# Kernel tuning notes

Measured on AMD Instinct MI355X. Metric: run time of the kernel, lower is better.

## Reference

```python
import jax, jax.numpy as jnp
from jax import lax
import numpy as np

D_MODEL = 256
NQ = 256          # nqueries / npoint
RADIUS = 0.3
NSAMPLE = 16
EPS = 1e-5


def _conv1d(x, W, b):  # x: (B,C,N), W: (O,C)
    return jnp.einsum('bcn,oc->bon', x, W) + b[None, :, None]


def _bn1d(x, g, be):  # train-mode batchnorm over (B, N)
    m = x.mean(axis=(0, 2), keepdims=True)
    v = x.var(axis=(0, 2), keepdims=True)
    return g[None, :, None] * (x - m) * lax.rsqrt(v + EPS) + be[None, :, None]


def _bn2d(x, g, be):  # x: (B,C,Q,S)
    m = x.mean(axis=(0, 2, 3), keepdims=True)
    v = x.var(axis=(0, 2, 3), keepdims=True)
    return g[None, :, None, None] * (x - m) * lax.rsqrt(v + EPS) + be[None, :, None, None]


def _fps(xyz, nq):
    # sequential farthest point sampling, starts at index 0 (matches CUDA impl)
    B, N, _ = xyz.shape

    def step(carry, _):
        dist, far = carry
        centroid = jnp.take_along_axis(xyz, far[:, None, None], axis=1)  # (B,1,3)
        d = jnp.sum((xyz - centroid) ** 2, axis=-1)                      # (B,N)
        dist = jnp.minimum(dist, d)
        nxt = jnp.argmax(dist, axis=-1).astype(jnp.int32)
        return (dist, nxt), far

    init = (jnp.full((B, N), 1e10, xyz.dtype), jnp.zeros((B,), jnp.int32))
    _, inds = lax.scan(step, init, None, length=nq)
    return inds.T  # (B,nq)


def _ball_query(query_xyz, xyz, radius, nsample):
    # query_xyz: (B,Q,3), xyz: (B,N,3) -> idx (B,Q,nsample) int32
    N = xyz.shape[1]
    d2 = jnp.sum((query_xyz[:, :, None, :] - xyz[:, None, :, :]) ** 2, axis=-1)  # (B,Q,N)
    within = d2 < radius * radius
    scores = jnp.where(within, jnp.arange(N, dtype=jnp.int32), jnp.int32(N))
    neg_top, _ = lax.top_k(-scores, nsample)          # nsample smallest scores, in order
    idx = -neg_top                                    # (B,Q,nsample)
    cnt = within.sum(axis=-1)                         # (B,Q)
    first = jnp.where(cnt > 0, idx[..., 0], 0)        # fill value (first neighbor, else 0)
    valid = jnp.arange(nsample) < cnt[..., None]
    return jnp.where(valid, idx, first[..., None])


def setup_inputs() -> dict:
    key = jax.random.key(0)
    ks = jax.random.split(key, 32)
    B, N, C = 16, 4096, D_MODEL
    s = 0.02
    inp = {
        'encode_xyz': jax.random.uniform(ks[0], (B, N, 3), jnp.float32),
        'encode_features': jax.random.normal(ks[1], (B, C, N), jnp.float32),
        # FFN_vote: conv1 -> bn -> relu -> conv2 -> bn -> relu -> conv3
        'W1': jax.random.normal(ks[2], (C, C), jnp.float32) * s,
        'b1': jnp.zeros((C,), jnp.float32),
        'g1': jnp.ones((C,), jnp.float32),
        'be1': jnp.zeros((C,), jnp.float32),
        'W2': jax.random.normal(ks[3], (C, C), jnp.float32) * s,
        'b2': jnp.zeros((C,), jnp.float32),
        'g2': jnp.ones((C,), jnp.float32),
        'be2': jnp.zeros((C,), jnp.float32),
        'W3': jax.random.normal(ks[4], (3 + C, C), jnp.float32) * s,
        'b3': jnp.zeros((3 + C,), jnp.float32),
        # SA module shared MLP (conv2d 1x1): (C+3)->C->C->C, each with BN2d
        'mW1': jax.random.normal(ks[5], (C, C + 3), jnp.float32) * s,
        'mb1': jnp.zeros((C,), jnp.float32),
        'mg1': jnp.ones((C,), jnp.float32),
        'mbe1': jnp.zeros((C,), jnp.float32),
        'mW2': jax.random.normal(ks[6], (C, C), jnp.float32) * s,
        'mb2': jnp.zeros((C,), jnp.float32),
        'mg2': jnp.ones((C,), jnp.float32),
        'mbe2': jnp.zeros((C,), jnp.float32),
        'mW3': jax.random.normal(ks[7], (C, C), jnp.float32) * s,
        'mb3': jnp.zeros((C,), jnp.float32),
        'mg3': jnp.ones((C,), jnp.float32),
        'mbe3': jnp.zeros((C,), jnp.float32),
    }
    return inp


def reference(encode_xyz, encode_features, W1, b1, g1, be1, W2, b2, g2, be2, W3, b3,
              mW1, mb1, mg1, mbe1, mW2, mb2, mg2, mbe2, mW3, mb3, mg3, mbe3):
    B, N, _ = encode_xyz.shape

    # FFN_vote
    h = jax.nn.relu(_bn1d(_conv1d(encode_features, W1, b1), g1, be1))
    h = jax.nn.relu(_bn1d(_conv1d(h, W2, b2), g2, be2))
    out = _conv1d(h, W3, b3)                      # (B, 3+C, N)

    coord_shift = jnp.clip(jax.nn.sigmoid(out[:, :3, :]), 0.1, 0.9)
    vote_xyz = encode_xyz + coord_shift.transpose(0, 2, 1) - 0.5   # (B,N,3)

    feat = encode_features + out[:, 3:, :]
    feat = feat / jnp.linalg.norm(feat, axis=1, keepdims=True)     # L2 normalize over C

    sample_inds = _fps(encode_xyz, NQ)                             # (B,NQ) int32

    # SA module: gather new centers from vote_xyz at FPS inds
    query_xyz = jnp.take_along_axis(vote_xyz, sample_inds[:, :, None], axis=1)  # (B,NQ,3)

    idx = _ball_query(query_xyz, vote_xyz, RADIUS, NSAMPLE)        # (B,NQ,NS)
    bidx = jnp.arange(B)[:, None, None]
    grouped_xyz = (vote_xyz[bidx, idx] - query_xyz[:, :, None, :]) / RADIUS  # (B,NQ,NS,3)
    grouped_feat = feat.transpose(0, 2, 1)[bidx, idx]                         # (B,NQ,NS,C)
    g = jnp.concatenate([grouped_xyz, grouped_feat], axis=-1)                 # (B,NQ,NS,3+C)
    g = g.transpose(0, 3, 1, 2)                                               # (B,3+C,NQ,NS)

    g = jax.nn.relu(_bn2d(jnp.einsum('bcqs,oc->boqs', g, mW1) + mb1[None, :, None, None], mg1, mbe1))
    g = jax.nn.relu(_bn2d(jnp.einsum('bcqs,oc->boqs', g, mW2) + mb2[None, :, None, None], mg2, mbe2))
    g = jax.nn.relu(_bn2d(jnp.einsum('bcqs,oc->boqs', g, mW3) + mb3[None, :, None, None], mg3, mbe3))
    query_features = jnp.max(g, axis=-1)                                      # (B,C,NQ)

    return vote_xyz, encode_xyz, sample_inds, query_xyz, query_features
```

## Files before the change

kernel.cpp:

```cpp
#include <hip/hip_runtime.h>
#include <math.h>

#define NPT 4096
#define NB 16

typedef short v8s __attribute__((ext_vector_type(8)));
typedef float v4f __attribute__((ext_vector_type(4)));

__device__ __forceinline__ float dist2e(float x, float y, float z,
                                        float cx, float cy, float cz) {
    float dx = __fsub_rn(x, cx), dy = __fsub_rn(y, cy), dz = __fsub_rn(z, cz);
    return __fadd_rn(__fadd_rn(__fmul_rn(dx, dx), __fmul_rn(dy, dy)), __fmul_rn(dz, dz));
}

__device__ __forceinline__ unsigned long long packdi(float v, int n) {
    return ((unsigned long long)__float_as_uint(v) << 32) |
           (unsigned long long)(0xFFFFFFFFu - (unsigned)n);
}

__device__ __forceinline__ unsigned short f2bf(float f) {
    unsigned u = __float_as_uint(f);
    u = u + 0x7FFFu + ((u >> 16) & 1u);
    return (unsigned short)(u >> 16);
}

__device__ __forceinline__ unsigned pk2(float a, float b) {
    unsigned r;
    asm("v_cvt_pk_bf16_f32 %0, %1, %2" : "=v"(r) : "v"(a), "v"(b));
    return r;
}

__device__ __forceinline__ uint2 split2(float a, float b) {
    unsigned h = pk2(a, b);
    float ra = __uint_as_float(h << 16);
    float rb = __uint_as_float(h & 0xFFFF0000u);
    unsigned l = pk2(a - ra, b - rb);
    return make_uint2(h, l);
}

template <int CTRL>
__device__ __forceinline__ float dpp_maxf(float v) {
    int o = __builtin_amdgcn_update_dpp(__float_as_int(v), __float_as_int(v),
                                        CTRL, 0xF, 0xF, false);
    return fmaxf(v, __int_as_float(o));
}
template <int CTRL>
__device__ __forceinline__ unsigned dpp_maxu(unsigned v) {
    unsigned o = (unsigned)__builtin_amdgcn_update_dpp((int)v, (int)v,
                                                       CTRL, 0xF, 0xF, false);
    return v > o ? v : o;
}

__device__ void fps_seg(const float* __restrict__ xyz, int b, int it0, int it1,
                        int* __restrict__ inds_i, float* __restrict__ inds_f,
                        float* __restrict__ dws, int* __restrict__ farws,
                        char* scr) {
    unsigned long long (*s_red)[4] = (unsigned long long (*)[4])scr;
    const int t = threadIdx.x;
    const int lane = t & 63, wid = t >> 6;
    const float* pb = xyz + (size_t)b * NPT * 3;
    float px[16], py[16], pz[16], d[16];
    #pragma unroll
    for (int j = 0; j < 16; ++j) {
        int p = j * 256 + t;
        px[j] = pb[p * 3 + 0];
        py[j] = pb[p * 3 + 1];
        pz[j] = pb[p * 3 + 2];
    }
    int far;
    if (it0 == 0) {
        #pragma unroll
        for (int j = 0; j < 16; ++j) d[j] = 1e10f;
        far = 0;
    } else {
        #pragma unroll
        for (int j = 0; j < 16; ++j) d[j] = dws[b * 4096 + j * 256 + t];
        far = farws[b];
    }
    for (int it = it0; it < it1; ++it) {
        const int par = it & 1;
        if (t == 0) { inds_i[it] = far; inds_f[it] = (float)far; }
        const float cx = pb[far * 3 + 0];
        const float cy = pb[far * 3 + 1];
        const float cz = pb[far * 3 + 2];
        d[0] = fminf(d[0], dist2e(px[0], py[0], pz[0], cx, cy, cz));
        unsigned long long best = packdi(d[0], t);
        #pragma unroll
        for (int j = 1; j < 16; ++j) {
            d[j] = fminf(d[j], dist2e(px[j], py[j], pz[j], cx, cy, cz));
            unsigned long long c = packdi(d[j], j * 256 + t);
            if (c > best) best = c;
        }
        const unsigned hi = (unsigned)(best >> 32);
        const unsigned lo = (unsigned)(best & 0xFFFFFFFFull);
        float m = __uint_as_float(hi);
        m = dpp_maxf<0x111>(m);
        m = dpp_maxf<0x112>(m);
        m = dpp_maxf<0x114>(m);
        m = dpp_maxf<0x118>(m);
        m = dpp_maxf<0x142>(m);
        m = dpp_maxf<0x143>(m);
        const unsigned mbits = (unsigned)__builtin_amdgcn_readlane(__float_as_int(m), 63);
        unsigned cand = (hi == mbits) ? lo : 0u;
        cand = dpp_maxu<0x111>(cand);
        cand = dpp_maxu<0x112>(cand);
        cand = dpp_maxu<0x114>(cand);
        cand = dpp_maxu<0x118>(cand);
        cand = dpp_maxu<0x142>(cand);
        cand = dpp_maxu<0x143>(cand);
        const unsigned wlo = (unsigned)__builtin_amdgcn_readlane((int)cand, 63);
        if (lane == 0)
            s_red[par][wid] = ((unsigned long long)mbits << 32) | (unsigned long long)wlo;
        __syncthreads();
        unsigned long long mm = s_red[par][0];
        if (s_red[par][1] > mm) mm = s_red[par][1];
        if (s_red[par][2] > mm) mm = s_red[par][2];
        if (s_red[par][3] > mm) mm = s_red[par][3];
        far = (int)(0xFFFFFFFFu - (unsigned)(mm & 0xFFFFFFFFull));
    }
    if (it1 < 256) {
        #pragma unroll
        for (int j = 0; j < 16; ++j) dws[b * 4096 + j * 256 + t] = d[j];
        if (t == 0) farws[b] = far;
    }
}

template <bool PRE_BN, bool STATS>
__global__ __launch_bounds__(256, 4)
void fgemm_k(const float* __restrict__ X,
             const unsigned short* __restrict__ Wh,
             const unsigned short* __restrict__ Wl,
             const float* __restrict__ bias,
             const float* __restrict__ scl, const float* __restrict__ sft,
             float* __restrict__ Y,
             float* __restrict__ psum, float* __restrict__ psqr,
             const float* __restrict__ xyz, int* __restrict__ sinds,
             float* __restrict__ inds_f, float* __restrict__ fpsd,
             int* __restrict__ fpsfar, int it0, int it1) {
    __shared__ __align__(16) unsigned short sBh[128 * 64];
    __shared__ __align__(16) unsigned short sBl[128 * 64];
    if (blockIdx.x < 16) {
        fps_seg(xyz, blockIdx.x, it0, it1, sinds + blockIdx.x * 256,
                inds_f + blockIdx.x * 256, fpsd, fpsfar, (char*)sBh);
        return;
    }
    int idx = blockIdx.x - 16;
    idx = (idx & 7) * 128 + (idx >> 3);
    const int b = idx >> 6, rem = idx & 63;
    const int nt = rem >> 1;
    const int n0 = nt * 128, o0 = (rem & 1) * 128;
    const int t = threadIdx.x;
    const int w = t >> 6, lane = t & 63;
    const int wm = (w >> 1) * 64, wn = (w & 1) * 64;
    const int lr = lane & 15, lk = lane >> 4;
    char* cBh = (char*)sBh;
    char* cBl = (char*)sBl;

    v4f acc[4][4];
    v4f zz = {0.f, 0.f, 0.f, 0.f};
    #pragma unroll
    for (int i = 0; i < 4; ++i)
        #pragma unroll
        for (int j = 0; j < 4; ++j) acc[i][j] = zz;

    const size_t aoff = (size_t)(o0 + wm + lr) * 256 + lk * 8;
    const unsigned short* pah = Wh + aoff;
    const unsigned short* pal = Wl + aoff;

    const int cblk = t >> 5, nq = t & 31;
    const float* xb = X + ((size_t)b * 256 + cblk * 8) * 4096 + n0 + nq * 4;

    #pragma unroll 1
    for (int ks = 0; ks < 4; ++ks) {
        const int k0 = ks * 64;
        v4f xv[8];
        #pragma unroll
        for (int i = 0; i < 8; ++i)
            xv[i] = *(const v4f*)(xb + (size_t)(k0 + i) * 4096);
        if (PRE_BN) {
            const v4f s0 = *(const v4f*)(scl + k0 + cblk * 8);
            const v4f s1 = *(const v4f*)(scl + k0 + cblk * 8 + 4);
            const v4f f0 = *(const v4f*)(sft + k0 + cblk * 8);
            const v4f f1 = *(const v4f*)(sft + k0 + cblk * 8 + 4);
            #pragma unroll
            for (int i = 0; i < 8; ++i) {
                const float si = (i < 4) ? s0[i] : s1[i - 4];
                const float fi = (i < 4) ? f0[i] : f1[i - 4];
                #pragma unroll
                for (int j = 0; j < 4; ++j)
                    xv[i][j] = fmaxf(fmaf(xv[i][j], si, fi), 0.f);
            }
        }
        __syncthreads();
        #pragma unroll
        for (int j = 0; j < 4; ++j) {
            const int n = nq * 4 + j;
            uint2 p0 = split2(xv[0][j], xv[1][j]);
            uint2 p1 = split2(xv[2][j], xv[3][j]);
            uint2 p2 = split2(xv[4][j], xv[5][j]);
            uint2 p3 = split2(xv[6][j], xv[7][j]);
            uint4 hh, ll;
            hh.x = p0.x; hh.y = p1.x; hh.z = p2.x; hh.w = p3.x;
            ll.x = p0.y; ll.y = p1.y; ll.z = p2.y; ll.w = p3.y;
            const int ad = n * 128 + ((cblk * 16) ^ ((n & 7) << 4));
            *(uint4*)(cBh + ad) = hh;
            *(uint4*)(cBl + ad) = ll;
        }
        __syncthreads();
        #pragma unroll
        for (int kb = 0; kb < 2; ++kb) {
            const int koff = kb * 64 + lk * 16;
            const int ka = k0 + kb * 32;
            v8s ahf[4], alf[4], bhf[4], blf[4];
            #pragma unroll
            for (int f = 0; f < 4; ++f) {
                ahf[f] = *(const v8s*)(pah + (size_t)f * 4096 + ka);
                alf[f] = *(const v8s*)(pal + (size_t)f * 4096 + ka);
                const int rn = wn + f * 16 + lr;
                const int bm = rn * 128 + (koff ^ ((rn & 7) << 4));
                bhf[f] = *(const v8s*)(cBh + bm);
                blf[f] = *(const v8s*)(cBl + bm);
            }
            #pragma unroll
            for (int fm = 0; fm < 4; ++fm)
                #pragma unroll
                for (int fn = 0; fn < 4; ++fn) {
                    acc[fm][fn] = __builtin_amdgcn_mfma_f32_16x16x32_bf16(
                        ahf[fm], bhf[fn], acc[fm][fn], 0, 0, 0);
                    acc[fm][fn] = __builtin_amdgcn_mfma_f32_16x16x32_bf16(
                        ahf[fm], blf[fn], acc[fm][fn], 0, 0, 0);
                    acc[fm][fn] = __builtin_amdgcn_mfma_f32_16x16x32_bf16(
                        alf[fm], bhf[fn], acc[fm][fn], 0, 0, 0);
                }
        }
    }

    float* Yb = Y + (size_t)b * 256 * 4096;
    const int gnt = b * 32 + nt;
    #pragma unroll
    for (int fm = 0; fm < 4; ++fm) {
        const int obase = o0 + wm + fm * 16 + lk * 4;
        float bv[4];
        #pragma unroll
        for (int j = 0; j < 4; ++j) bv[j] = bias[obase + j];
        float ssr[4] = {0.f, 0.f, 0.f, 0.f}, qqr[4] = {0.f, 0.f, 0.f, 0.f};
        #pragma unroll
        for (int fn = 0; fn < 4; ++fn) {
            const int gn = n0 + wn + fn * 16 + lr;
            #pragma unroll
            for (int j = 0; j < 4; ++j) {
                const float yv = acc[fm][fn][j] + bv[j];
                Yb[(size_t)(obase + j) * 4096 + gn] = yv;
                ssr[j] += yv; qqr[j] += yv * yv;
            }
        }
        if (STATS) {
            #pragma unroll
            for (int j = 0; j < 4; ++j) {
                #pragma unroll
                for (int off = 1; off < 16; off <<= 1) {
                    ssr[j] += __shfl_xor(ssr[j], off, 64);
                    qqr[j] += __shfl_xor(qqr[j], off, 64);
                }
            }
            if (lr == 0) {
                const int col = gnt * 2 + (w & 1);
                #pragma unroll
                for (int j = 0; j < 4; ++j) {
                    psum[(size_t)(obase + j) * 1024 + col] = ssr[j];
                    psqr[(size_t)(obase + j) * 1024 + col] = qqr[j];
                }
            }
        }
    }
}

__global__ __launch_bounds__(256)
void prepw_k(const float* __restrict__ W1, const float* __restrict__ W2,
             const float* __restrict__ W3, unsigned short* __restrict__ h1,
             unsigned short* __restrict__ l1, unsigned short* __restrict__ h2,
             unsigned short* __restrict__ l2, unsigned short* __restrict__ h3,
             unsigned short* __restrict__ l3) {
    const int o = blockIdx.x & 255, which = blockIdx.x >> 8, t = threadIdx.x;
    float v;
    unsigned short* ph;
    unsigned short* pl;
    if (which == 0) { v = W1[(size_t)o * 256 + t]; ph = h1; pl = l1; }
    else if (which == 1) { v = W2[(size_t)o * 256 + t]; ph = h2; pl = l2; }
    else { v = W3[(size_t)(o + 3) * 256 + t]; ph = h3; pl = l3; }
    unsigned short hu = f2bf(v);
    float rv = v - __uint_as_float((unsigned)hu << 16);
    ph[o * 256 + t] = hu;
    pl[o * 256 + t] = f2bf(rv);
}

__global__ __launch_bounds__(64)
void fin_k(const float* __restrict__ psum, const float* __restrict__ psqr,
           const float* __restrict__ g, const float* __restrict__ be,
           float* __restrict__ scl, float* __restrict__ sft, int npart) {
    const int c = blockIdx.x, t = threadIdx.x;
    const float4* ps = (const float4*)(psum + (size_t)c * 1024);
    const float4* pq = (const float4*)(psqr + (size_t)c * 1024);
    float s = 0.f, q = 0.f;
    for (int r = t; r < (npart >> 2); r += 64) {
        float4 a = ps[r]; s += a.x + a.y + a.z + a.w;
        float4 b2 = pq[r]; q += b2.x + b2.y + b2.z + b2.w;
    }
    #pragma unroll
    for (int sh = 32; sh; sh >>= 1) {
        s += __shfl_down(s, (unsigned)sh, 64);
        q += __shfl_down(q, (unsigned)sh, 64);
    }
    if (t == 0) {
        float mean = s * (1.f / 65536.f);
        float var = q * (1.f / 65536.f) - mean * mean;
        float sc = g[c] / sqrtf(var + 1e-5f);
        scl[c] = sc;
        sft[c] = be[c] - mean * sc;
    }
}

__global__ __launch_bounds__(256)
void prep_k(const float* __restrict__ mW1, const float* __restrict__ mW2,
            const float* __restrict__ mW3, unsigned short* __restrict__ W1p,
            unsigned short* __restrict__ W2p, unsigned short* __restrict__ W3p) {
    const int o = blockIdx.x & 255, which = blockIdx.x >> 8, t = threadIdx.x;
    if (which == 0) {
        W1p[o * 320 + t] = f2bf(mW1[o * 259 + 3 + t]);
        if (t < 64) {
            float v = (t < 3) ? mW1[o * 259 + t] : 0.f;
            W1p[o * 320 + 256 + t] = f2bf(v);
        }
    } else if (which == 1) {
        W2p[o * 256 + t] = f2bf(mW2[o * 256 + t]);
    } else {
        W3p[o * 256 + t] = f2bf(mW3[o * 256 + t]);
    }
}

__global__ __launch_bounds__(256)
void votefeat_k(const float* __restrict__ OUT, const float* __restrict__ Y2,
                const float* __restrict__ xyz, const float* __restrict__ feats,
                const float* __restrict__ scl2, const float* __restrict__ sft2,
                const float* __restrict__ W3, const float* __restrict__ b3,
                float* __restrict__ vote_out, float* __restrict__ xyz_out,
                unsigned short* __restrict__ featT,
                int* __restrict__ sinds, float* __restrict__ inds_f,
                float* __restrict__ fpsd, int* __restrict__ fpsfar,
                int it0, int it1) {
    __shared__ float tile[32 * 257];
    __shared__ float ssb[32 * 9];
    __shared__ float rn[32];
    __shared__ float sW3[768];
    __shared__ float dred[3][8][33];
    if (blockIdx.x < 16) {
        fps_seg(xyz, blockIdx.x, it0, it1, sinds + blockIdx.x * 256,
                inds_f + blockIdx.x * 256, fpsd, fpsfar, (char*)tile);
        return;
    }
    const int blk = blockIdx.x - 16;
    const int b = blk >> 7, n0 = (blk & 127) * 32;
    const int t = threadIdx.x;
    const int nl = t & 31, co = t >> 5;
    const float* Ob = OUT + (size_t)b * 256 * NPT;
    const float* Yb = Y2 + (size_t)b * 256 * NPT;
    #pragma unroll
    for (int r = 0; r < 3; ++r) sW3[r * 256 + t] = W3[r * 256 + t];
    __syncthreads();
    float ss = 0.f, d0 = 0.f, d1 = 0.f, d2 = 0.f;
    #pragma unroll 4
    for (int ci = 0; ci < 32; ++ci) {
        const int c = ci * 8 + co;
        const size_t coff = (size_t)c * NPT + n0 + nl;
        float v = feats[(size_t)b * 256 * NPT + coff] + Ob[coff];
        tile[nl * 257 + c] = v;
        ss += v * v;
        float h = fmaxf(fmaf(Yb[coff], scl2[c], sft2[c]), 0.f);
        d0 = fmaf(h, sW3[c], d0);
        d1 = fmaf(h, sW3[256 + c], d1);
        d2 = fmaf(h, sW3[512 + c], d2);
    }
    ssb[nl * 9 + co] = ss;
    dred[0][co][nl] = d0;
    dred[1][co][nl] = d1;
    dred[2][co][nl] = d2;
    __syncthreads();
    if (t < 32) {
        float s = 0.f;
        #pragma unroll
        for (int j = 0; j < 8; ++j) s += ssb[t * 9 + j];
        rn[t] = 1.0f / sqrtf(s);
    }
    __syncthreads();
    for (int p = 0; p < 32; ++p)
        featT[((size_t)b * NPT + n0 + p) * 256 + t] = f2bf(tile[p * 257 + t] * rn[p]);
    if (t < 96) {
        const int r = t >> 5, p = t & 31;
        float d = b3[r];
        #pragma unroll
        for (int j = 0; j < 8; ++j) d += dred[r][j][p];
        float sig = 1.f / (1.f + expf(-d));
        sig = fminf(fmaxf(sig, 0.1f), 0.9f);
        const size_t gi = ((size_t)b * NPT + n0 + p) * 3 + r;
        const float e = xyz[gi];
        vote_out[gi] = e + sig - 0.5f;
        xyz_out[gi] = e;
    }
}

__global__ __launch_bounds__(64)
void bq_k(const float* __restrict__ vote, const int* __restrict__ sinds,
          float* __restrict__ qxyz_out, int* __restrict__ idx_out) {
    const int bq = blockIdx.x;
    const int b = bq >> 8;
    const int lane = threadIdx.x;
    __shared__ int s_idx[16];
    const int si = sinds[bq];
    const float* vb = vote + (size_t)b * NPT * 3;
    const float qx = vb[si * 3 + 0], qy = vb[si * 3 + 1], qz = vb[si * 3 + 2];
    if (lane < 3) qxyz_out[bq * 3 + lane] = vb[si * 3 + lane];
    int cnt = 0;
    for (int cb = 0; cb < 64 && cnt < 16; ++cb) {
        int n = cb * 64 + lane;
        float x = vb[n * 3], y = vb[n * 3 + 1], z = vb[n * 3 + 2];
        float d2 = dist2e(x, y, z, qx, qy, qz);
        unsigned long long m = __ballot(d2 < 0.09f);
        while (m && cnt < 16) {
            int bit = __builtin_ctzll(m);
            s_idx[cnt] = cb * 64 + bit;
            ++cnt;
            m &= m - 1;
        }
    }
    __syncthreads();
    if (lane < 16) {
        int v = (lane < cnt) ? s_idx[lane] : (cnt > 0 ? s_idx[0] : 0);
        idx_out[bq * 16 + lane] = v;
    }
}

__global__ __launch_bounds__(256)
void group_k(const unsigned short* __restrict__ featT, const float* __restrict__ vote,
             const float* __restrict__ qxyz, const int* __restrict__ idxs,
             unsigned short* __restrict__ Gt) {
    const int bq = blockIdx.x;
    const int b = bq >> 8, q = bq & 255;
    const int t = threadIdx.x;
    __shared__ int s_i[16];
    __shared__ float s_q[3];
    if (t < 16) s_i[t] = idxs[bq * 16 + t];
    if (t < 3) s_q[t] = qxyz[bq * 3 + t];
    __syncthreads();
    const int s = t >> 4, part = t & 15;
    const int i = s_i[s];
    const size_t nrow = (size_t)b * 4096 + q * 16 + s;
    const uint4* src = (const uint4*)(featT + ((size_t)b * NPT + i) * 256 + part * 16);
    uint4* dst = (uint4*)(Gt + nrow * 320 + part * 16);
    dst[0] = src[0];
    dst[1] = src[1];
    for (int c = 259 + part; c < 320; c += 16) Gt[nrow * 320 + c] = 0;
    if (part < 3) {
        float v = (vote[((size_t)b * NPT + i) * 3 + part] - s_q[part]) * (1.f / 0.3f);
        Gt[nrow * 320 + 256 + part] = f2bf(v);
    }
}

__device__ __forceinline__ unsigned bnpair(unsigned u, float sl, float sh,
                                           float fl, float fh) {
    float lo = __uint_as_float(u << 16);
    float hi = __uint_as_float(u & 0xFFFF0000u);
    lo = fmaxf(fmaf(lo, sl, fl), 0.f);
    hi = fmaxf(fmaf(hi, sh, fh), 0.f);
    unsigned r;
    asm("v_cvt_pk_bf16_f32 %0, %1, %2" : "=v"(r) : "v"(lo), "v"(hi));
    return r;
}

template <int KPAD, bool BNSTAGE, bool EPIMAX>
__global__ __launch_bounds__(256, 2)
void mgemm_k(const unsigned short* __restrict__ Wb,
             const unsigned short* __restrict__ Xt,
             const float* __restrict__ bias,
             const float* __restrict__ scl, const float* __restrict__ sft,
             unsigned short* __restrict__ Yt, float* __restrict__ rmax,
             float* __restrict__ psum, float* __restrict__ psqr) {
    __shared__ __align__(16) unsigned short sA[128 * 64];
    __shared__ __align__(16) unsigned short sB[128 * 64];
    char* cA = (char*)sA;
    char* cB = (char*)sB;
    const int t = threadIdx.x;
    const int n0 = blockIdx.x * 128, o0 = blockIdx.y * 128;
    const int w = t >> 6, lane = t & 63;
    const int wm = (w >> 1) * 64, wn = (w & 1) * 64;
    const int lr = lane & 15, lk = lane >> 4;

    v4f acc[4][4];
    v4f zz = {0.f, 0.f, 0.f, 0.f};
    #pragma unroll
    for (int i = 0; i < 4; ++i)
        #pragma unroll
        for (int j = 0; j < 4; ++j) acc[i][j] = zz;

    const int ra = t >> 1, kc = (t & 1) * 32;
    const unsigned short* asrc = Wb + (size_t)(o0 + ra) * KPAD + kc;
    const unsigned short* bsrc = Xt + (size_t)(n0 + ra) * KPAD + kc;
    const int nk = KPAD / 64;

    for (int ks = 0; ks < nk; ++ks) {
        const int k0 = ks * 64;
        uint4 av[4], bv[4];
        #pragma unroll
        for (int i = 0; i < 4; ++i) av[i] = *(const uint4*)(asrc + k0 + 8 * i);
        #pragma unroll
        for (int i = 0; i < 4; ++i) bv[i] = *(const uint4*)(bsrc + k0 + 8 * i);
        if constexpr (BNSTAGE) {
            #pragma unroll
            for (int i = 0; i < 4; ++i) {
                const int kk = k0 + kc + 8 * i;
                float4 s0 = *(const float4*)(scl + kk);
                float4 s1 = *(const float4*)(scl + kk + 4);
                float4 f0 = *(const float4*)(sft + kk);
                float4 f1 = *(const float4*)(sft + kk + 4);
                bv[i].x = bnpair(bv[i].x, s0.x, s0.y, f0.x, f0.y);
                bv[i].y = bnpair(bv[i].y, s0.z, s0.w, f0.z, f0.w);
                bv[i].z = bnpair(bv[i].z, s1.x, s1.y, f1.x, f1.y);
                bv[i].w = bnpair(bv[i].w, s1.z, s1.w, f1.z, f1.w);
            }
        }
        __syncthreads();
        #pragma unroll
        for (int i = 0; i < 4; ++i) {
            const int kb2 = (kc + 8 * i) * 2;
            *(uint4*)(cA + ra * 128 + (kb2 ^ ((ra & 7) << 4))) = av[i];
            *(uint4*)(cB + ra * 128 + (kb2 ^ ((ra & 7) << 4))) = bv[i];
        }
        __syncthreads();
        #pragma unroll
        for (int kb = 0; kb < 2; ++kb) {
            const int koff = (kb * 32 + lk * 8) * 2;
            v8s af[4], bf[4];
            #pragma unroll
            for (int f = 0; f < 4; ++f) {
                const int rm = wm + f * 16 + lr;
                af[f] = *(const v8s*)(cA + rm * 128 + (koff ^ ((rm & 7) << 4)));
                const int rn = wn + f * 16 + lr;
                bf[f] = *(const v8s*)(cB + rn * 128 + (koff ^ ((rn & 7) << 4)));
            }
            #pragma unroll
            for (int fm = 0; fm < 4; ++fm)
                #pragma unroll
                for (int fn = 0; fn < 4; ++fn)
                    acc[fm][fn] = __builtin_amdgcn_mfma_f32_16x16x32_bf16(
                        af[fm], bf[fn], acc[fm][fn], 0, 0, 0);
        }
    }

    const int bx = blockIdx.x;
    #pragma unroll
    for (int fm = 0; fm < 4; ++fm) {
        const int obase = o0 + wm + fm * 16 + lk * 4;
        const float4 bv4 = *(const float4*)(bias + obase);
        float s0 = 0.f, s1 = 0.f, s2 = 0.f, s3 = 0.f;
        float q0 = 0.f, q1 = 0.f, q2 = 0.f, q3 = 0.f;
        #pragma unroll
        for (int fn = 0; fn < 4; ++fn) {
            float y0 = acc[fm][fn][0] + bv4.x;
            float y1 = acc[fm][fn][1] + bv4.y;
            float y2 = acc[fm][fn][2] + bv4.z;
            float y3 = acc[fm][fn][3] + bv4.w;
            s0 += y0; s1 += y1; s2 += y2; s3 += y3;
            q0 += y0 * y0; q1 += y1 * y1; q2 += y2 * y2; q3 += y3 * y3;
            if constexpr (!EPIMAX) {
                unsigned p0, p1;
                asm("v_cvt_pk_bf16_f32 %0, %1, %2" : "=v"(p0) : "v"(y0), "v"(y1));
                asm("v_cvt_pk_bf16_f32 %0, %1, %2" : "=v"(p1) : "v"(y2), "v"(y3));
                const int gn = n0 + wn + fn * 16 + lr;
                *(uint2*)(Yt + (size_t)gn * 256 + obase) = make_uint2(p0, p1);
            } else {
                float m0 = y0, m1 = y1, m2 = y2, m3 = y3;
                #pragma unroll
                for (int off = 1; off < 16; off <<= 1) {
                    m0 = fmaxf(m0, __shfl_xor(m0, off, 64));
                    m1 = fmaxf(m1, __shfl_xor(m1, off, 64));
                    m2 = fmaxf(m2, __shfl_xor(m2, off, 64));
                    m3 = fmaxf(m3, __shfl_xor(m3, off, 64));
                }
                if (lr == 0) {
                    const int gq = (n0 + wn + fn * 16) >> 4;
                    const int bb = gq >> 8, qq = gq & 255;
                    float* rp = rmax + ((size_t)bb * 256 + obase) * 256 + qq;
                    rp[0] = m0; rp[256] = m1; rp[512] = m2; rp[768] = m3;
                }
            }
        }
        #pragma unroll
        for (int off = 1; off < 16; off <<= 1) {
            s0 += __shfl_xor(s0, off, 64); q0 += __shfl_xor(q0, off, 64);
            s1 += __shfl_xor(s1, off, 64); q1 += __shfl_xor(q1, off, 64);
            s2 += __shfl_xor(s2, off, 64); q2 += __shfl_xor(q2, off, 64);
            s3 += __shfl_xor(s3, off, 64); q3 += __shfl_xor(q3, off, 64);
        }
        if (lr == 0) {
            const int col = bx * 2 + (w & 1);
            psum[(size_t)(obase + 0) * 1024 + col] = s0;
            psum[(size_t)(obase + 1) * 1024 + col] = s1;
            psum[(size_t)(obase + 2) * 1024 + col] = s2;
            psum[(size_t)(obase + 3) * 1024 + col] = s3;
            psqr[(size_t)(obase + 0) * 1024 + col] = q0;
            psqr[(size_t)(obase + 1) * 1024 + col] = q1;
            psqr[(size_t)(obase + 2) * 1024 + col] = q2;
            psqr[(size_t)(obase + 3) * 1024 + col] = q3;
        }
    }
}

__global__ __launch_bounds__(256)
void qf_k(const float* __restrict__ rmax, const float* __restrict__ scl,
          const float* __restrict__ sft, float* __restrict__ out) {
    const int g = blockIdx.x * 256 + threadIdx.x;
    const int c = (g >> 8) & 255;
    out[g] = fmaxf(fmaf(rmax[g], scl[c], sft[c]), 0.f);
}

extern "C" void kernel_launch(void* const* d_in, const int* in_sizes, int n_in,
                              void* d_out, int out_size, void* d_ws, size_t ws_size,
                              hipStream_t stream) {
    const float* xyz   = (const float*)d_in[0];
    const float* feats = (const float*)d_in[1];
    const float* W1 = (const float*)d_in[2];
    const float* b1 = (const float*)d_in[3];
    const float* g1 = (const float*)d_in[4];
    const float* be1 = (const float*)d_in[5];
    const float* W2 = (const float*)d_in[6];
    const float* b2 = (const float*)d_in[7];
    const float* g2 = (const float*)d_in[8];
    const float* be2 = (const float*)d_in[9];
    const float* W3 = (const float*)d_in[10];
    const float* b3 = (const float*)d_in[11];
    const float* mW1 = (const float*)d_in[12];
    const float* mb1 = (const float*)d_in[13];
    const float* mg1 = (const float*)d_in[14];
    const float* mbe1 = (const float*)d_in[15];
    const float* mW2 = (const float*)d_in[16];
    const float* mb2 = (const float*)d_in[17];
    const float* mg2 = (const float*)d_in[18];
    const float* mbe2 = (const float*)d_in[19];
    const float* mW3 = (const float*)d_in[20];
    const float* mb3 = (const float*)d_in[21];
    const float* mg3 = (const float*)d_in[22];
    const float* mbe3 = (const float*)d_in[23];

    float* out_vote = (float*)d_out;
    float* out_xyz = out_vote + 196608;
    float* out_inds = out_xyz + 196608;
    float* out_q = out_inds + 4096;
    float* out_qf = out_q + 12288;

    float* ws = (float*)d_ws;
    float* A      = ws;
    float* Bb     = A + 16973824;
    float* Ft     = Bb + 16777216;
    float* rawmax = Ft + 8388608;
    float* psum   = rawmax + 1048576;
    float* psqr   = psum + 262144;
    float* st     = psqr + 262144;
    float* fpsd   = st + 2560;
    float* wbase  = fpsd + 65536;
    unsigned short* Wb1 = (unsigned short*)wbase;
    unsigned short* Wb2 = Wb1 + 81920;
    unsigned short* Wb3 = Wb2 + 65536;
    int* sinds  = (int*)(Wb3 + 65536);
    int* bidx   = sinds + 4096;
    int* fpsfar = bidx + 65536;

    unsigned short* Gt  = (unsigned short*)A;
    unsigned short* Y1t = (unsigned short*)Bb;
    unsigned short* featT = (unsigned short*)Ft;
    unsigned short* Y2t = (unsigned short*)Ft;

    unsigned short* Wf1h = (unsigned short*)rawmax;
    unsigned short* Wf1l = Wf1h + 65536;
    unsigned short* Wf2h = Wf1l + 65536;
    unsigned short* Wf2l = Wf2h + 65536;
    unsigned short* Wf3h = Wf2l + 65536;
    unsigned short* Wf3l = Wf3h + 65536;

    prep_k<<<768, 256, 0, stream>>>(mW1, mW2, mW3, Wb1, Wb2, Wb3);
    prepw_k<<<768, 256, 0, stream>>>(W1, W2, W3, Wf1h, Wf1l, Wf2h, Wf2l, Wf3h, Wf3l);

    fgemm_k<false, true><<<1040, 256, 0, stream>>>(
        feats, Wf1h, Wf1l, b1, nullptr, nullptr, A, psum, psqr,
        xyz, sinds, out_inds, fpsd, fpsfar, 0, 64);
    fin_k<<<256, 64, 0, stream>>>(psum, psqr, g1, be1, st + 0, st + 256, 1024);
    fgemm_k<true, true><<<1040, 256, 0, stream>>>(
        A, Wf2h, Wf2l, b2, st + 0, st + 256, Bb, psum, psqr,
        xyz, sinds, out_inds, fpsd, fpsfar, 64, 128);
    fin_k<<<256, 64, 0, stream>>>(psum, psqr, g2, be2, st + 512, st + 768, 1024);
    fgemm_k<true, false><<<1040, 256, 0, stream>>>(
        Bb, Wf3h, Wf3l, b3 + 3, st + 512, st + 768, A, nullptr, nullptr,
        xyz, sinds, out_inds, fpsd, fpsfar, 128, 192);

    votefeat_k<<<2064, 256, 0, stream>>>(A, Bb, xyz, feats, st + 512, st + 768,
                                         W3, b3, out_vote, out_xyz, featT,
                                         sinds, out_inds, fpsd, fpsfar, 192, 256);
    bq_k<<<4096, 64, 0, stream>>>(out_vote, sinds, out_q, bidx);
    group_k<<<4096, 256, 0, stream>>>(featT, out_vote, out_q, bidx, Gt);

    mgemm_k<320, false, false><<<dim3(512, 2), 256, 0, stream>>>(
        Wb1, Gt, mb1, nullptr, nullptr, Y1t, nullptr, psum, psqr);
    fin_k<<<256, 64, 0, stream>>>(psum, psqr, mg1, mbe1, st + 1024, st + 1280, 1024);
    mgemm_k<256, true, false><<<dim3(512, 2), 256, 0, stream>>>(
        Wb2, Y1t, mb2, st + 1024, st + 1280, Y2t, nullptr, psum, psqr);
    fin_k<<<256, 64, 0, stream>>>(psum, psqr, mg2, mbe2, st + 1536, st + 1792, 1024);
    mgemm_k<256, true, true><<<dim3(512, 2), 256, 0, stream>>>(
        Wb3, Y2t, mb3, st + 1536, st + 1792, nullptr, rawmax, psum, psqr);
    fin_k<<<256, 64, 0, stream>>>(psum, psqr, mg3, mbe3, st + 2048, st + 2304, 1024);
    qf_k<<<4096, 256, 0, stream>>>(rawmax, st + 2048, st + 2304, out_qf);
}
```

Measured before the change: 565.0 us.

## Prefetch next K-tile global loads into registers during MFMA compute in GEMM kernels

```diff
diff --git a/kernel.cpp b/kernel.cpp
--- a/kernel.cpp
+++ b/kernel.cpp
@@ -36,6 +36,22 @@
     float rb = __uint_as_float(h & 0xFFFF0000u);
     unsigned l = pk2(a - ra, b - rb);
     return make_uint2(h, l);
+}
+
+__device__ __forceinline__ void bn8(v4f* xv, const float* __restrict__ scl,
+                                    const float* __restrict__ sft, int base) {
+    const v4f s0 = *(const v4f*)(scl + base);
+    const v4f s1 = *(const v4f*)(scl + base + 4);
+    const v4f f0 = *(const v4f*)(sft + base);
+    const v4f f1 = *(const v4f*)(sft + base + 4);
+    #pragma unroll
+    for (int i = 0; i < 8; ++i) {
+        const float si = (i < 4) ? s0[i] : s1[i - 4];
+        const float fi = (i < 4) ? f0[i] : f1[i - 4];
+        #pragma unroll
+        for (int j = 0; j < 4; ++j)
+            xv[i][j] = fmaxf(fmaf(xv[i][j], si, fi), 0.f);
+    }
 }
 
 template <int CTRL>
@@ -170,35 +186,23 @@
     const int cblk = t >> 5, nq = t & 31;
     const float* xb = X + ((size_t)b * 256 + cblk * 8) * 4096 + n0 + nq * 4;
 
-    #pragma unroll 1
+    v4f cur[8];
+    #pragma unroll
+    for (int i = 0; i < 8; ++i)
+        cur[i] = *(const v4f*)(xb + (size_t)i * 4096);
+    if (PRE_BN) bn8(cur, scl, sft, cblk * 8);
+
+    #pragma unroll
     for (int ks = 0; ks < 4; ++ks) {
         const int k0 = ks * 64;
-        v4f xv[8];
-        #pragma unroll
-        for (int i = 0; i < 8; ++i)
-            xv[i] = *(const v4f*)(xb + (size_t)(k0 + i) * 4096);
-        if (PRE_BN) {
-            const v4f s0 = *(const v4f*)(scl + k0 + cblk * 8);
-            const v4f s1 = *(const v4f*)(scl + k0 + cblk * 8 + 4);
-            const v4f f0 = *(const v4f*)(sft + k0 + cblk * 8);
-            const v4f f1 = *(const v4f*)(sft + k0 + cblk * 8 + 4);
-            #pragma unroll
-            for (int i = 0; i < 8; ++i) {
-                const float si = (i < 4) ? s0[i] : s1[i - 4];
-                const float fi = (i < 4) ? f0[i] : f1[i - 4];
-                #pragma unroll
-                for (int j = 0; j < 4; ++j)
-                    xv[i][j] = fmaxf(fmaf(xv[i][j], si, fi), 0.f);
-            }
-        }
         __syncthreads();
         #pragma unroll
         for (int j = 0; j < 4; ++j) {
             const int n = nq * 4 + j;
-            uint2 p0 = split2(xv[0][j], xv[1][j]);
-            uint2 p1 = split2(xv[2][j], xv[3][j]);
-            uint2 p2 = split2(xv[4][j], xv[5][j]);
-            uint2 p3 = split2(xv[6][j], xv[7][j]);
+            uint2 p0 = split2(cur[0][j], cur[1][j]);
+            uint2 p1 = split2(cur[2][j], cur[3][j]);
+            uint2 p2 = split2(cur[4][j], cur[5][j]);
+            uint2 p3 = split2(cur[6][j], cur[7][j]);
             uint4 hh, ll;
             hh.x = p0.x; hh.y = p1.x; hh.z = p2.x; hh.w = p3.x;
             ll.x = p0.y; ll.y = p1.y; ll.z = p2.y; ll.w = p3.y;
@@ -207,6 +211,12 @@
             *(uint4*)(cBl + ad) = ll;
         }
         __syncthreads();
+        if (ks < 3) {
+            #pragma unroll
+            for (int i = 0; i < 8; ++i)
+                cur[i] = *(const v4f*)(xb + (size_t)(k0 + 64 + i) * 4096);
+            if (PRE_BN) bn8(cur, scl, sft, k0 + 64 + cblk * 8);
+        }
         #pragma unroll
         for (int kb = 0; kb < 2; ++kb) {
             const int koff = kb * 64 + lk * 16;
@@ -504,29 +514,30 @@
     const int ra = t >> 1, kc = (t & 1) * 32;
     const unsigned short* asrc = Wb + (size_t)(o0 + ra) * KPAD + kc;
     const unsigned short* bsrc = Xt + (size_t)(n0 + ra) * KPAD + kc;
-    const int nk = KPAD / 64;
-
+    constexpr int nk = KPAD / 64;
+
+    uint4 av[4], bv[4];
+    #pragma unroll
+    for (int i = 0; i < 4; ++i) av[i] = *(const uint4*)(asrc + 8 * i);
+    #pragma unroll
+    for (int i = 0; i < 4; ++i) bv[i] = *(const uint4*)(bsrc + 8 * i);
+    if constexpr (BNSTAGE) {
+        #pragma unroll
+        for (int i = 0; i < 4; ++i) {
+            const int kk = kc + 8 * i;
+            float4 s0 = *(const float4*)(scl + kk);
+            float4 s1 = *(const float4*)(scl + kk + 4);
+            float4 f0 = *(const float4*)(sft + kk);
+            float4 f1 = *(const float4*)(sft + kk + 4);
+            bv[i].x = bnpair(bv[i].x, s0.x, s0.y, f0.x, f0.y);
+            bv[i].y = bnpair(bv[i].y, s0.z, s0.w, f0.z, f0.w);
+            bv[i].z = bnpair(bv[i].z, s1.x, s1.y, f1.x, f1.y);
+            bv[i].w = bnpair(bv[i].w, s1.z, s1.w, f1.z, f1.w);
+        }
+    }
+
+    #pragma unroll
     for (int ks = 0; ks < nk; ++ks) {
-        const int k0 = ks * 64;
-        uint4 av[4], bv[4];
-        #pragma unroll
-        for (int i = 0; i < 4; ++i) av[i] = *(const uint4*)(asrc + k0 + 8 * i);
-        #pragma unroll
-        for (int i = 0; i < 4; ++i) bv[i] = *(const uint4*)(bsrc + k0 + 8 * i);
-        if constexpr (BNSTAGE) {
-            #pragma unroll
-            for (int i = 0; i < 4; ++i) {
-                const int kk = k0 + kc + 8 * i;
-                float4 s0 = *(const float4*)(scl + kk);
-                float4 s1 = *(const float4*)(scl + kk + 4);
-                float4 f0 = *(const float4*)(sft + kk);
-                float4 f1 = *(const float4*)(sft + kk + 4);
-                bv[i].x = bnpair(bv[i].x, s0.x, s0.y, f0.x, f0.y);
-                bv[i].y = bnpair(bv[i].y, s0.z, s0.w, f0.z, f0.w);
-                bv[i].z = bnpair(bv[i].z, s1.x, s1.y, f1.x, f1.y);
-                bv[i].w = bnpair(bv[i].w, s1.z, s1.w, f1.z, f1.w);
-            }
-        }
         __syncthreads();
         #pragma unroll
         for (int i = 0; i < 4; ++i) {
@@ -535,6 +546,27 @@
             *(uint4*)(cB + ra * 128 + (kb2 ^ ((ra & 7) << 4))) = bv[i];
         }
         __syncthreads();
+        if (ks + 1 < nk) {
+            const int k1 = (ks + 1) * 64;
+            #pragma unroll
+            for (int i = 0; i < 4; ++i) av[i] = *(const uint4*)(asrc + k1 + 8 * i);
+            #pragma unroll
+            for (int i = 0; i < 4; ++i) bv[i] = *(const uint4*)(bsrc + k1 + 8 * i);
+            if constexpr (BNSTAGE) {
+                #pragma unroll
+                for (int i = 0; i < 4; ++i) {
+                    const int kk = k1 + kc + 8 * i;
+                    float4 s0 = *(const float4*)(scl + kk);
+                    float4 s1 = *(const float4*)(scl + kk + 4);
+                    float4 f0 = *(const float4*)(sft + kk);
+                    float4 f1 = *(const float4*)(sft + kk + 4);
+                    bv[i].x = bnpair(bv[i].x, s0.x, s0.y, f0.x, f0.y);
+                    bv[i].y = bnpair(bv[i].y, s0.z, s0.w, f0.z, f0.w);
+                    bv[i].z = bnpair(bv[i].z, s1.x, s1.y, f1.x, f1.y);
+                    bv[i].w = bnpair(bv[i].w, s1.z, s1.w, f1.z, f1.w);
+                }
+            }
+        }
         #pragma unroll
         for (int kb = 0; kb < 2; ++kb) {
             const int koff = (kb * 32 + lk * 8) * 2;
```

Result: no change. 565.3 us (+0.1%).
